# Performance work log

Hardware: AMD Instinct MI355X
Metric: run time of the kernel (lower is better)

Reference implementation:

```python
import jax, jax.numpy as jnp
import numpy as np

NUM_HEADS = 12

def _get_rel_pos(q_size, k_size, rel_pos):
    # rel_pos already has shape (2*max(q,k)-1, head_dim) -> no resize needed
    q_coords = jnp.arange(q_size)[:, None] * max(k_size / q_size, 1.0)
    k_coords = jnp.arange(k_size)[None, :] * max(q_size / k_size, 1.0)
    rel = (q_coords - k_coords + (k_size - 1) * max(q_size / k_size, 1.0)).astype(jnp.int32)
    return rel_pos[rel.reshape(-1)].reshape(q_size, k_size, -1)  # (q, k, head_dim)


def setup_inputs() -> dict:
    key = jax.random.key(0)
    ks = jax.random.split(key, 7)
    B, H, W, C = 1, 64, 64, 768
    head_dim = C // NUM_HEADS
    return {
        "x": jax.random.normal(ks[0], (B, H, W, C), jnp.float32),
        "qkv_w": jax.random.normal(ks[1], (C, 3 * C), jnp.float32) * 0.02,
        "qkv_b": jax.random.normal(ks[2], (3 * C,), jnp.float32) * 0.02,
        "rel_pos_h": jax.random.normal(ks[3], (2 * H - 1, head_dim), jnp.float32) * 0.02,
        "rel_pos_w": jax.random.normal(ks[4], (2 * W - 1, head_dim), jnp.float32) * 0.02,
        "proj_w": jax.random.normal(ks[5], (C, C), jnp.float32) * 0.02,
        "proj_b": jax.random.normal(ks[6], (C,), jnp.float32) * 0.02,
    }


def reference(x, qkv_w, qkv_b, rel_pos_h, rel_pos_w, proj_w, proj_b):
    B, H, W, C = x.shape
    nh = NUM_HEADS
    hd = C // nh
    scale = hd ** (-0.5)
    S = H * W

    qkv = x @ qkv_w + qkv_b                              # (B,H,W,3C)
    qkv = qkv.reshape(B, S, 3, nh, hd).transpose(2, 0, 3, 1, 4).reshape(3, B * nh, S, hd)
    q, k, v = qkv[0], qkv[1], qkv[2]                     # (B*nh, S, hd)

    attn = jnp.einsum('bqd,bkd->bqk', q * scale, k)      # (B*nh, S, S)

    rh = _get_rel_pos(H, H, rel_pos_h)                   # (H,H,hd)
    rw = _get_rel_pos(W, W, rel_pos_w)                   # (W,W,hd)
    r_q = q.reshape(B * nh, H, W, hd)
    rel_h = jnp.einsum('bhwc,hkc->bhwk', r_q, rh)        # (B*nh,H,W,H)
    rel_w = jnp.einsum('bhwc,wkc->bhwk', r_q, rw)        # (B*nh,H,W,W)
    attn = (attn.reshape(B * nh, H, W, H, W)
            + rel_h[:, :, :, :, None]
            + rel_w[:, :, :, None, :]).reshape(B * nh, S, S)

    attn = jax.nn.softmax(attn, axis=-1)
    out = jnp.einsum('bqk,bkd->bqd', attn, v)            # (B*nh, S, hd)
    out = out.reshape(B, nh, H, W, hd).transpose(0, 2, 3, 1, 4).reshape(B, H, W, C)
    return out @ proj_w + proj_b
```

## Files before the change

### kernel.cpp

```cpp
#include <hip/hip_runtime.h>
#include <hip/hip_bf16.h>

#define S_TOK 4096
#define CDIM  768
#define N3C   2304
#define NH    12
#define HD    64

#define LOG2E 1.44269504f

typedef __attribute__((ext_vector_type(8))) short short8;
typedef __attribute__((ext_vector_type(4))) short short4v;
typedef __attribute__((ext_vector_type(4))) float float4v;
typedef __attribute__((ext_vector_type(4))) unsigned uint4v;

__device__ __forceinline__ float b2f(short s) {
    return __uint_as_float(((unsigned)(unsigned short)s) << 16);
}
__device__ __forceinline__ short f2b(float f) {
    unsigned u = __float_as_uint(f);
    unsigned r = (u + 0x7FFFu + ((u >> 16) & 1u)) >> 16;
    return (short)r;
}

#if __has_builtin(__builtin_amdgcn_exp2f)
#define EXP2F __builtin_amdgcn_exp2f
#else
#define EXP2F exp2f
#endif

__device__ __forceinline__ unsigned pack_trunc(float a, float b) {
    return __builtin_amdgcn_perm(__float_as_uint(b), __float_as_uint(a), 0x07060302u);
}

__device__ __forceinline__ short8 u4_to_s8(unsigned a, unsigned b, unsigned c, unsigned d) {
    union { uint4v u; short8 s; } t;
    t.u = (uint4v){a, b, c, d};
    return t.s;
}

__device__ __forceinline__ void load_lds16(const void* g, void* l) {
    __builtin_amdgcn_global_load_lds(
        (const __attribute__((address_space(1))) unsigned int*)g,
        (__attribute__((address_space(3))) unsigned int*)l, 16, 0, 0);
}

__global__ __launch_bounds__(256) void cast_bf16_kernel(
    const float* __restrict__ in, short* __restrict__ out, int n4)
{
    int i = blockIdx.x * 256 + threadIdx.x;
    if (i >= n4) return;
    float4 v = ((const float4*)in)[i];
    short4v o4 = { f2b(v.x), f2b(v.y), f2b(v.z), f2b(v.w) };
    *(short4v*)&out[(size_t)i * 4] = o4;
}

__global__ __launch_bounds__(256) void transpose_cast_kernel(
    const float* __restrict__ in, short* __restrict__ out, int R, int C)
{
    __shared__ float t[64][65];
    const int tid = threadIdx.x;
    const int c0 = blockIdx.x * 64, r0 = blockIdx.y * 64;
    const int li = tid >> 6;
    const int lj = tid & 63;
#pragma unroll
    for (int p = 0; p < 16; ++p) {
        int i = p * 4 + li;
        t[i][lj] = in[(size_t)(r0 + i) * C + c0 + lj];
    }
    __syncthreads();
#pragma unroll
    for (int p = 0; p < 16; ++p) {
        int i = p * 4 + li;
        out[(size_t)(c0 + i) * R + r0 + lj] = f2b(t[lj][i]);
    }
}

#define GEMM_CORE(A_, Bt_)                                                     \
    __shared__ __align__(16) short a_s[128][72];                               \
    __shared__ __align__(16) short b_s[128][72];                               \
    const int tid  = threadIdx.x;                                              \
    const int m0 = blockIdx.y * 128;                                           \
    const int n0 = blockIdx.x * 128;                                           \
    const int lane = tid & 63, w = tid >> 6;                                   \
    const int l15 = lane & 15, quad = lane >> 4;                               \
    const int wr = w >> 1, wc = w & 1;                                         \
    const int srow = tid >> 1;                                                 \
    const int scol = (tid & 1) * 32;                                           \
    float4v acc[4][4];                                                         \
    _Pragma("unroll")                                                          \
    for (int i = 0; i < 4; ++i)                                                \
        _Pragma("unroll")                                                      \
        for (int j = 0; j < 4; ++j) acc[i][j] = (float4v){0.f,0.f,0.f,0.f};    \
    for (int k0 = 0; k0 < 768; k0 += 64) {                                     \
        __syncthreads();                                                       \
        const short* ga = A_ + (size_t)(m0 + srow) * 768 + k0 + scol;          \
        const short* gb = Bt_ + (size_t)(n0 + srow) * 768 + k0 + scol;         \
        _Pragma("unroll")                                                      \
        for (int v = 0; v < 4; ++v) {                                          \
            *(uint4*)&a_s[srow][scol + v*8] = *(const uint4*)(ga + v*8);       \
            *(uint4*)&b_s[srow][scol + v*8] = *(const uint4*)(gb + v*8);       \
        }                                                                      \
        __syncthreads();                                                       \
        _Pragma("unroll")                                                      \
        for (int kk = 0; kk < 64; kk += 32) {                                  \
            short8 af[4], bfr[4];                                              \
            _Pragma("unroll")                                                  \
            for (int i = 0; i < 4; ++i)                                        \
                af[i] = *(const short8*)&a_s[wr*64 + i*16 + l15][kk + quad*8]; \
            _Pragma("unroll")                                                  \
            for (int j = 0; j < 4; ++j)                                        \
                bfr[j] = *(const short8*)&b_s[wc*64 + j*16 + l15][kk + quad*8];\
            _Pragma("unroll")                                                  \
            for (int i = 0; i < 4; ++i)                                        \
                _Pragma("unroll")                                              \
                for (int j = 0; j < 4; ++j)                                    \
                    acc[i][j] = __builtin_amdgcn_mfma_f32_16x16x32_bf16(       \
                        af[i], bfr[j], acc[i][j], 0, 0, 0);                    \
        }                                                                      \
    }

__global__ __launch_bounds__(256) void gemm_qkv_mfma(
    const short* __restrict__ A, const short* __restrict__ Bt,
    const float* __restrict__ bias,
    short* __restrict__ Qb, short* __restrict__ Kb, short* __restrict__ Vt)
{
    GEMM_CORE(A, Bt)

    const int sec = n0 / CDIM;
    float bj[4];
#pragma unroll
    for (int j = 0; j < 4; ++j) bj[j] = bias[n0 + wc*64 + j*16 + l15];

    if (sec < 2) {
        short* dst = (sec == 0) ? Qb : Kb;
#pragma unroll
        for (int i = 0; i < 4; ++i)
#pragma unroll
            for (int j = 0; j < 4; ++j) {
                const int nn = (n0 + wc*64 + j*16 + l15) % CDIM;
                const int head = nn >> 6, d = nn & 63;
#pragma unroll
                for (int r = 0; r < 4; ++r) {
                    const int s = m0 + wr*64 + i*16 + quad*4 + r;
                    dst[((size_t)head * S_TOK + s) * HD + d] = f2b(acc[i][j][r] + bj[j]);
                }
            }
    } else {
#pragma unroll
        for (int i = 0; i < 4; ++i)
#pragma unroll
            for (int j = 0; j < 4; ++j) {
                const int nn = (n0 + wc*64 + j*16 + l15) % CDIM;
                const int head = nn >> 6, d = nn & 63;
                const int sbase = m0 + wr*64 + i*16 + quad*4;
                short4v v4;
#pragma unroll
                for (int r = 0; r < 4; ++r) v4[r] = f2b(acc[i][j][r] + bj[j]);
                *(short4v*)&Vt[((size_t)head * HD + d) * S_TOK + sbase] = v4;
            }
    }
}

__global__ __launch_bounds__(256) void gemm_proj_mfma(
    const short* __restrict__ A, const short* __restrict__ Bt,
    const float* __restrict__ bias, float* __restrict__ out)
{
    GEMM_CORE(A, Bt)

    float bj[4];
#pragma unroll
    for (int j = 0; j < 4; ++j) bj[j] = bias[n0 + wc*64 + j*16 + l15];

#pragma unroll
    for (int i = 0; i < 4; ++i)
#pragma unroll
        for (int j = 0; j < 4; ++j) {
            const int n = n0 + wc*64 + j*16 + l15;
#pragma unroll
            for (int r = 0; r < 4; ++r) {
                const int s = m0 + wr*64 + i*16 + quad*4 + r;
                out[(size_t)s * CDIM + n] = acc[i][j][r] + bj[j];
            }
        }
}

__global__ __launch_bounds__(256) void rel_mfma_kernel(
    const short* __restrict__ Qb, const float* __restrict__ rph,
    const float* __restrict__ rpw, short* __restrict__ Relh,
    short* __restrict__ Relw)
{
    __shared__ __align__(16) short q_s [64][72];
    __shared__ __align__(16) short rh_s[64][72];
    __shared__ __align__(16) short rw_s[128][72];

    const int tid  = threadIdx.x;
    const int y    = blockIdx.x;
    const int head = blockIdx.y;
    const int s0   = y * 64;
    const int w = tid >> 6, lane = tid & 63;
    const int l15 = lane & 15, quad = lane >> 4;
    const int srow = tid >> 2;
    const int scol = (tid & 3) << 4;

    {
        const uint4* g = (const uint4*)(Qb + ((size_t)head * S_TOK + s0 + srow) * HD + scol);
        *(uint4*)&q_s[srow][scol]     = g[0];
        *(uint4*)&q_s[srow][scol + 8] = g[1];
    }
    {
        const float* g = rph + (size_t)(y + srow) * HD + scol;
        short tmp[16];
#pragma unroll
        for (int i = 0; i < 16; i += 4) {
            float4 v = *(const float4*)(g + i);
            tmp[i] = f2b(v.x); tmp[i+1] = f2b(v.y); tmp[i+2] = f2b(v.z); tmp[i+3] = f2b(v.w);
        }
        *(short8*)&rh_s[srow][scol]     = *(short8*)&tmp[0];
        *(short8*)&rh_s[srow][scol + 8] = *(short8*)&tmp[8];
    }
#pragma unroll
    for (int half = 0; half < 2; ++half) {
        const int row = srow + half * 64;
        const int rr  = row > 126 ? 126 : row;
        const float* g = rpw + (size_t)rr * HD + scol;
        short tmp[16];
#pragma unroll
        for (int i = 0; i < 16; i += 4) {
            float4 v = *(const float4*)(g + i);
            tmp[i] = f2b(v.x); tmp[i+1] = f2b(v.y); tmp[i+2] = f2b(v.z); tmp[i+3] = f2b(v.w);
        }
        *(short8*)&rw_s[row][scol]     = *(short8*)&tmp[0];
        *(short8*)&rw_s[row][scol + 8] = *(short8*)&tmp[8];
    }
    __syncthreads();

    const short8 qa0 = *(const short8*)&q_s[w * 16 + l15][quad * 8];
    const short8 qa1 = *(const short8*)&q_s[w * 16 + l15][32 + quad * 8];

#pragma unroll
    for (int ct = 0; ct < 4; ++ct) {
        const int jj = ct * 16 + l15;
        short8 b0 = *(const short8*)&rh_s[jj][quad * 8];
        short8 b1 = *(const short8*)&rh_s[jj][32 + quad * 8];
        float4v z = (float4v){0.f, 0.f, 0.f, 0.f};
        z = __builtin_amdgcn_mfma_f32_16x16x32_bf16(qa0, b0, z, 0, 0, 0);
        z = __builtin_amdgcn_mfma_f32_16x16x32_bf16(qa1, b1, z, 0, 0, 0);
        const int ky = 63 - jj;
#pragma unroll
        for (int r = 0; r < 4; ++r) {
            const int q = w * 16 + quad * 4 + r;
            Relh[((size_t)head * S_TOK + s0 + q) * HD + ky] = f2b(z[r] * LOG2E);
        }
    }

#pragma unroll
    for (int ct = 0; ct < 8; ++ct) {
        const int j = ct * 16 + l15;
        short8 b0 = *(const short8*)&rw_s[j][quad * 8];
        short8 b1 = *(const short8*)&rw_s[j][32 + quad * 8];
        float4v z = (float4v){0.f, 0.f, 0.f, 0.f};
        z = __builtin_amdgcn_mfma_f32_16x16x32_bf16(qa0, b0, z, 0, 0, 0);
        z = __builtin_amdgcn_mfma_f32_16x16x32_bf16(qa1, b1, z, 0, 0, 0);
#pragma unroll
        for (int r = 0; r < 4; ++r) {
            const int q  = w * 16 + quad * 4 + r;
            const int kx = q + 63 - j;
            if (kx >= 0 && kx < 64)
                Relw[((size_t)head * S_TOK + s0 + q) * HD + kx] = f2b(z[r] * LOG2E);
        }
    }
}

__global__ __launch_bounds__(256, 3) void flash_kernel(
    const short* __restrict__ Qb, const short* __restrict__ Kb,
    const short* __restrict__ Vt, const short* __restrict__ Relh,
    const short* __restrict__ Relw, short* __restrict__ attn_b)
{
    __shared__ __align__(16) short lds_s[24576];

    const int tid  = threadIdx.x;
    const int head = blockIdx.y;
    const int s0   = blockIdx.x * 64;
    const int w    = tid >> 6, lane = tid & 63;
    const int l15  = lane & 15, quad = lane >> 4;
    const int ph   = w >> 1;
    const int qh   = w & 1;

    const float C1 = 0.125f * LOG2E;

    const int lj = lane >> 3;
    const int sl = (lane & 7) ^ lj;
    const int kf0 = (lj & 3) + ((lj & 4) << 1) + qh * 32;

    const short* pKs = Kb + (size_t)head * S_TOK * HD
                     + (size_t)(ph * 32 * 64 + kf0) * HD + sl * 8;
    const short* pVs = Vt + ((size_t)head * HD + qh * 32 + lj) * S_TOK
                     + ph * 32 * 64 + sl * 8;

    short* lk0 = &lds_s[(ph * 2 + 0) << 12] + qh * 32 * 64;
    short* lk1 = &lds_s[(ph * 2 + 1) << 12] + qh * 32 * 64;
    short* lv  = &lds_s[16384 + (ph << 12)] + qh * 32 * 64;
    const short* krd0 = &lds_s[(ph * 2 + 0) << 12];
    const short* krd1 = &lds_s[(ph * 2 + 1) << 12];
    const short* vrd  = &lds_s[16384 + (ph << 12)];

    const int roff0 = (quad ^ (l15 & 7)) << 4;
    const int roff1 = roff0 ^ 64;

    short8 qb[2][2];
#pragma unroll
    for (int qt = 0; qt < 2; ++qt) {
        const short* qrow = Qb + ((size_t)head * S_TOK + s0 + qh * 32 + qt * 16 + l15) * HD;
        qb[qt][0] = *(const short8*)(qrow + quad * 8);
        qb[qt][1] = *(const short8*)(qrow + 32 + quad * 8);
    }

    float rwv[2][4][4];
#pragma unroll
    for (int qt = 0; qt < 2; ++qt) {
        const short* rwrow = Relw + ((size_t)head * S_TOK + s0 + qh * 32 + qt * 16 + l15) * HD;
#pragma unroll
        for (int kt = 0; kt < 4; ++kt) {
            const int base = ((kt & 1) << 2) | ((kt >> 1) << 5);
            short4v v = *(const short4v*)(rwrow + base + quad * 8);
#pragma unroll
            for (int r = 0; r < 4; ++r) rwv[qt][kt][r] = b2f(v[r]);
        }
    }

    const short* rhrow0 = Relh + ((size_t)head * S_TOK + s0 + qh * 32 + l15) * HD;
    const short* rhrow1 = rhrow0 + 16 * HD;

    short8 aones;
#pragma unroll
    for (int j = 0; j < 8; ++j) aones[j] = (short)0x3F80;

    float4v od[2][4];
#pragma unroll
    for (int qt = 0; qt < 2; ++qt)
#pragma unroll
        for (int dt = 0; dt < 4; ++dt) od[qt][dt] = (float4v){0.f, 0.f, 0.f, 0.f};
    float4v dq0 = (float4v){0.f, 0.f, 0.f, 0.f};
    float4v dq1 = (float4v){0.f, 0.f, 0.f, 0.f};

    load_lds16(pKs,        lk0);
    load_lds16(pKs + 1024, lk0 + 8  * 64);
    load_lds16(pKs + 256,  lk0 + 16 * 64);
    load_lds16(pKs + 1280, lk0 + 24 * 64);
    __syncthreads();

    for (int t = 0; t < 32; ++t) {
        const int cur = t & 1;
        const short* krd = cur ? krd1 : krd0;
        short* lkn = cur ? lk0 : lk1;

        load_lds16(pVs,               lv);
        load_lds16(pVs + 8  * S_TOK,  lv + 8  * 64);
        load_lds16(pVs + 16 * S_TOK,  lv + 16 * 64);
        load_lds16(pVs + 24 * S_TOK,  lv + 24 * 64);
        if (t < 31) {
            const short* pk = pKs + 4096;
            load_lds16(pk,        lkn);
            load_lds16(pk + 1024, lkn + 8  * 64);
            load_lds16(pk + 256,  lkn + 16 * 64);
            load_lds16(pk + 1280, lkn + 24 * 64);
        }
        pKs += 4096;
        pVs += 64;

        const int c = ph * 32 + t;
        const float rhc0 = b2f(rhrow0[c]);
        const float rhc1 = b2f(rhrow1[c]);

        unsigned pkk[2][8];
#pragma unroll
        for (int kt = 0; kt < 4; ++kt) {
            const char* krp = (const char*)(krd + (kt * 16 + l15) * 64);
            const short8 ka0 = *(const short8*)(krp + roff0);
            const short8 ka1 = *(const short8*)(krp + roff1);
            {
                float4v z = (float4v){0.f, 0.f, 0.f, 0.f};
                z = __builtin_amdgcn_mfma_f32_16x16x32_bf16(ka0, qb[0][0], z, 0, 0, 0);
                z = __builtin_amdgcn_mfma_f32_16x16x32_bf16(ka1, qb[0][1], z, 0, 0, 0);
                float p0 = EXP2F(C1 * z[0] + (rhc0 + rwv[0][kt][0]));
                float p1 = EXP2F(C1 * z[1] + (rhc0 + rwv[0][kt][1]));
                float p2 = EXP2F(C1 * z[2] + (rhc0 + rwv[0][kt][2]));
                float p3 = EXP2F(C1 * z[3] + (rhc0 + rwv[0][kt][3]));
                pkk[0][kt * 2]     = pack_trunc(p0, p1);
                pkk[0][kt * 2 + 1] = pack_trunc(p2, p3);
            }
            {
                float4v z = (float4v){0.f, 0.f, 0.f, 0.f};
                z = __builtin_amdgcn_mfma_f32_16x16x32_bf16(ka0, qb[1][0], z, 0, 0, 0);
                z = __builtin_amdgcn_mfma_f32_16x16x32_bf16(ka1, qb[1][1], z, 0, 0, 0);
                float p0 = EXP2F(C1 * z[0] + (rhc1 + rwv[1][kt][0]));
                float p1 = EXP2F(C1 * z[1] + (rhc1 + rwv[1][kt][1]));
                float p2 = EXP2F(C1 * z[2] + (rhc1 + rwv[1][kt][2]));
                float p3 = EXP2F(C1 * z[3] + (rhc1 + rwv[1][kt][3]));
                pkk[1][kt * 2]     = pack_trunc(p0, p1);
                pkk[1][kt * 2 + 1] = pack_trunc(p2, p3);
            }
        }
        const short8 pb00 = u4_to_s8(pkk[0][0], pkk[0][1], pkk[0][2], pkk[0][3]);
        const short8 pb01 = u4_to_s8(pkk[0][4], pkk[0][5], pkk[0][6], pkk[0][7]);
        const short8 pb10 = u4_to_s8(pkk[1][0], pkk[1][1], pkk[1][2], pkk[1][3]);
        const short8 pb11 = u4_to_s8(pkk[1][4], pkk[1][5], pkk[1][6], pkk[1][7]);

        __syncthreads();

#pragma unroll
        for (int dt = 0; dt < 4; ++dt) {
            const char* vrp = (const char*)(vrd + (dt * 16 + l15) * 64);
            const short8 va0 = *(const short8*)(vrp + roff0);
            const short8 va1 = *(const short8*)(vrp + roff1);
            od[0][dt] = __builtin_amdgcn_mfma_f32_16x16x32_bf16(va0, pb00, od[0][dt], 0, 0, 0);
            od[0][dt] = __builtin_amdgcn_mfma_f32_16x16x32_bf16(va1, pb01, od[0][dt], 0, 0, 0);
            od[1][dt] = __builtin_amdgcn_mfma_f32_16x16x32_bf16(va0, pb10, od[1][dt], 0, 0, 0);
            od[1][dt] = __builtin_amdgcn_mfma_f32_16x16x32_bf16(va1, pb11, od[1][dt], 0, 0, 0);
        }
        dq0 = __builtin_amdgcn_mfma_f32_16x16x32_bf16(aones, pb00, dq0, 0, 0, 0);
        dq0 = __builtin_amdgcn_mfma_f32_16x16x32_bf16(aones, pb01, dq0, 0, 0, 0);
        dq1 = __builtin_amdgcn_mfma_f32_16x16x32_bf16(aones, pb10, dq1, 0, 0, 0);
        dq1 = __builtin_amdgcn_mfma_f32_16x16x32_bf16(aones, pb11, dq1, 0, 0, 0);

        __syncthreads();
    }

    float* cf = (float*)lds_s;
    if (ph == 1) {
#pragma unroll
        for (int qt = 0; qt < 2; ++qt)
#pragma unroll
            for (int dt = 0; dt < 4; ++dt) {
                float* dst = &cf[((((qh * 2 + qt) * 4 + dt) * 16) + quad * 4) * 16 + l15];
#pragma unroll
                for (int r = 0; r < 4; ++r) dst[r * 16] = od[qt][dt][r];
            }
        if (quad == 0) {
            cf[4096 + (qh * 2 + 0) * 16 + l15] = dq0[0];
            cf[4096 + (qh * 2 + 1) * 16 + l15] = dq1[0];
        }
    }
    __syncthreads();
    if (ph == 0) {
#pragma unroll
        for (int qt = 0; qt < 2; ++qt) {
            const float dtot = ((qt == 0) ? dq0[0] : dq1[0])
                             + cf[4096 + (qh * 2 + qt) * 16 + l15];
            const float inv = 1.f / dtot;
            short* outp = attn_b + (size_t)(s0 + qh * 32 + qt * 16 + l15) * CDIM + head * HD;
#pragma unroll
            for (int dt = 0; dt < 4; ++dt) {
                const float* src = &cf[((((qh * 2 + qt) * 4 + dt) * 16) + quad * 4) * 16 + l15];
                short4v o4;
#pragma unroll
                for (int r = 0; r < 4; ++r)
                    o4[r] = f2b((od[qt][dt][r] + src[r * 16]) * inv);
                *(short4v*)(outp + dt * 16 + quad * 4) = o4;
            }
        }
    }
}

extern "C" void kernel_launch(void* const* d_in, const int* in_sizes, int n_in,
                              void* d_out, int out_size, void* d_ws, size_t ws_size,
                              hipStream_t stream)
{
    const float* x    = (const float*)d_in[0];
    const float* qkvw = (const float*)d_in[1];
    const float* qkvb = (const float*)d_in[2];
    const float* rph  = (const float*)d_in[3];
    const float* rpw  = (const float*)d_in[4];
    const float* pw   = (const float*)d_in[5];
    const float* pb   = (const float*)d_in[6];
    float* out = (float*)d_out;

    const size_t HSD = (size_t)NH * S_TOK * HD;
    short* xb     = (short*)d_ws;
    short* wt     = xb + (size_t)S_TOK * CDIM;
    short* pwt    = wt + (size_t)N3C * CDIM;
    short* Qb     = pwt + (size_t)CDIM * CDIM;
    short* Kb     = Qb + HSD;
    short* Vt     = Kb + HSD;
    short* Relh   = Vt + HSD;
    short* Relw   = Relh + HSD;
    short* attn_b = Relw + HSD;

    cast_bf16_kernel<<<S_TOK * CDIM / 4 / 256, 256, 0, stream>>>(x, xb, S_TOK * CDIM / 4);
    transpose_cast_kernel<<<dim3(N3C / 64, CDIM / 64), 256, 0, stream>>>(qkvw, wt, CDIM, N3C);
    transpose_cast_kernel<<<dim3(CDIM / 64, CDIM / 64), 256, 0, stream>>>(pw, pwt, CDIM, CDIM);

    gemm_qkv_mfma<<<dim3(N3C / 128, S_TOK / 128), 256, 0, stream>>>(
        xb, wt, qkvb, Qb, Kb, Vt);
    rel_mfma_kernel<<<dim3(64, NH), 256, 0, stream>>>(Qb, rph, rpw, Relh, Relw);
    flash_kernel<<<dim3(64, NH), 256, 0, stream>>>(Qb, Kb, Vt, Relh, Relw, attn_b);
    gemm_proj_mfma<<<dim3(CDIM / 128, S_TOK / 128), 256, 0, stream>>>(
        attn_b, pwt, pb, out);
}
```

Measured before the change: 224.2 us.

## Use direct-to-LDS swizzled GEMM loads, transpose Relh, prefetch bias, set MFMA priority

The shared GEMM core now fills LDS with direct global-to-LDS 16-byte loads (load_lds16) into an unpadded tile, using an XOR swizzle on the read offsets to avoid bank conflicts. The rel kernel writes the height bias transposed (head, ky, token), so it can store vectorized 4-element chunks. The flash kernel prefetches the next iteration's height-bias value so the load overlaps the current tile's compute. It also raises wave priority around the PV MFMA block. This mixes several independent changes, and correctness depends on the load_lds16 helper and the swizzle mapping matching the read side.

```diff
diff --git a/kernel.cpp b/kernel.cpp
--- a/kernel.cpp
+++ b/kernel.cpp
@@ -77,16 +77,22 @@
 }
 
 #define GEMM_CORE(A_, Bt_)                                                     \
-    __shared__ __align__(16) short a_s[128][72];                               \
-    __shared__ __align__(16) short b_s[128][72];                               \
+    __shared__ __align__(16) short a_s[128][64];                               \
+    __shared__ __align__(16) short b_s[128][64];                               \
     const int tid  = threadIdx.x;                                              \
     const int m0 = blockIdx.y * 128;                                           \
     const int n0 = blockIdx.x * 128;                                           \
     const int lane = tid & 63, w = tid >> 6;                                   \
     const int l15 = lane & 15, quad = lane >> 4;                               \
     const int wr = w >> 1, wc = w & 1;                                         \
-    const int srow = tid >> 1;                                                 \
-    const int scol = (tid & 1) * 32;                                           \
+    const int roff0 = (quad ^ (l15 & 7)) << 4;                                 \
+    const int roff1 = roff0 ^ 64;                                              \
+    const int srow0 = w * 8 + (lane >> 3);                                     \
+    const int sslot = (lane & 7) ^ ((lane >> 3) & 7);                          \
+    const short* ga = A_ + (size_t)(m0 + srow0) * 768 + sslot * 8;             \
+    const short* gb = Bt_ + (size_t)(n0 + srow0) * 768 + sslot * 8;            \
+    short* la = &a_s[w * 8][0];                                                \
+    short* lb = &b_s[w * 8][0];                                                \
     float4v acc[4][4];                                                         \
     _Pragma("unroll")                                                          \
     for (int i = 0; i < 4; ++i)                                                \
@@ -94,23 +100,22 @@
         for (int j = 0; j < 4; ++j) acc[i][j] = (float4v){0.f,0.f,0.f,0.f};    \
     for (int k0 = 0; k0 < 768; k0 += 64) {                                     \
         __syncthreads();                                                       \
-        const short* ga = A_ + (size_t)(m0 + srow) * 768 + k0 + scol;          \
-        const short* gb = Bt_ + (size_t)(n0 + srow) * 768 + k0 + scol;         \
         _Pragma("unroll")                                                      \
-        for (int v = 0; v < 4; ++v) {                                          \
-            *(uint4*)&a_s[srow][scol + v*8] = *(const uint4*)(ga + v*8);       \
-            *(uint4*)&b_s[srow][scol + v*8] = *(const uint4*)(gb + v*8);       \
+        for (int i = 0; i < 4; ++i) {                                          \
+            load_lds16(ga + (size_t)i * (32 * 768) + k0, la + i * 32 * 64);    \
+            load_lds16(gb + (size_t)i * (32 * 768) + k0, lb + i * 32 * 64);    \
         }                                                                      \
         __syncthreads();                                                       \
         _Pragma("unroll")                                                      \
         for (int kk = 0; kk < 64; kk += 32) {                                  \
+            const int roff = kk ? roff1 : roff0;                               \
             short8 af[4], bfr[4];                                              \
             _Pragma("unroll")                                                  \
             for (int i = 0; i < 4; ++i)                                        \
-                af[i] = *(const short8*)&a_s[wr*64 + i*16 + l15][kk + quad*8]; \
+                af[i] = *(const short8*)((const char*)&a_s[wr*64 + i*16 + l15][0] + roff); \
             _Pragma("unroll")                                                  \
             for (int j = 0; j < 4; ++j)                                        \
-                bfr[j] = *(const short8*)&b_s[wc*64 + j*16 + l15][kk + quad*8];\
+                bfr[j] = *(const short8*)((const char*)&b_s[wc*64 + j*16 + l15][0] + roff); \
             _Pragma("unroll")                                                  \
             for (int i = 0; i < 4; ++i)                                        \
                 _Pragma("unroll")                                              \
@@ -187,7 +192,7 @@
 
 __global__ __launch_bounds__(256) void rel_mfma_kernel(
     const short* __restrict__ Qb, const float* __restrict__ rph,
-    const float* __restrict__ rpw, short* __restrict__ Relh,
+    const float* __restrict__ rpw, short* __restrict__ RelhT,
     short* __restrict__ Relw)
 {
     __shared__ __align__(16) short q_s [64][72];
@@ -247,11 +252,10 @@
         z = __builtin_amdgcn_mfma_f32_16x16x32_bf16(qa0, b0, z, 0, 0, 0);
         z = __builtin_amdgcn_mfma_f32_16x16x32_bf16(qa1, b1, z, 0, 0, 0);
         const int ky = 63 - jj;
-#pragma unroll
-        for (int r = 0; r < 4; ++r) {
-            const int q = w * 16 + quad * 4 + r;
-            Relh[((size_t)head * S_TOK + s0 + q) * HD + ky] = f2b(z[r] * LOG2E);
-        }
+        short4v o4;
+#pragma unroll
+        for (int r = 0; r < 4; ++r) o4[r] = f2b(z[r] * LOG2E);
+        *(short4v*)&RelhT[((size_t)head * HD + ky) * S_TOK + s0 + w * 16 + quad * 4] = o4;
     }
 
 #pragma unroll
@@ -274,7 +278,7 @@
 
 __global__ __launch_bounds__(256, 3) void flash_kernel(
     const short* __restrict__ Qb, const short* __restrict__ Kb,
-    const short* __restrict__ Vt, const short* __restrict__ Relh,
+    const short* __restrict__ Vt, const short* __restrict__ RelhT,
     const short* __restrict__ Relw, short* __restrict__ attn_b)
 {
     __shared__ __align__(16) short lds_s[24576];
@@ -329,8 +333,9 @@
         }
     }
 
-    const short* rhrow0 = Relh + ((size_t)head * S_TOK + s0 + qh * 32 + l15) * HD;
-    const short* rhrow1 = rhrow0 + 16 * HD;
+    const short* rhbase = RelhT + (size_t)head * HD * S_TOK + s0 + qh * 32 + l15;
+    float rhc0 = b2f(rhbase[(size_t)(ph * 32) * S_TOK]);
+    float rhc1 = b2f(rhbase[(size_t)(ph * 32) * S_TOK + 16]);
 
     short8 aones;
 #pragma unroll
@@ -369,9 +374,11 @@
         pKs += 4096;
         pVs += 64;
 
-        const int c = ph * 32 + t;
-        const float rhc0 = b2f(rhrow0[c]);
-        const float rhc1 = b2f(rhrow1[c]);
+        short rhn0, rhn1;
+        if (t < 31) {
+            rhn0 = rhbase[(size_t)(ph * 32 + t + 1) * S_TOK];
+            rhn1 = rhbase[(size_t)(ph * 32 + t + 1) * S_TOK + 16];
+        }
 
         unsigned pkk[2][8];
 #pragma unroll
@@ -409,6 +416,7 @@
 
         __syncthreads();
 
+        __builtin_amdgcn_s_setprio(1);
 #pragma unroll
         for (int dt = 0; dt < 4; ++dt) {
             const char* vrp = (const char*)(vrd + (dt * 16 + l15) * 64);
@@ -423,7 +431,12 @@
         dq0 = __builtin_amdgcn_mfma_f32_16x16x32_bf16(aones, pb01, dq0, 0, 0, 0);
         dq1 = __builtin_amdgcn_mfma_f32_16x16x32_bf16(aones, pb10, dq1, 0, 0, 0);
         dq1 = __builtin_amdgcn_mfma_f32_16x16x32_bf16(aones, pb11, dq1, 0, 0, 0);
-
+        __builtin_amdgcn_s_setprio(0);
+
+        if (t < 31) {
+            rhc0 = b2f(rhn0);
+            rhc1 = b2f(rhn1);
+        }
         __syncthreads();
     }
 
@@ -483,8 +496,8 @@
     short* Qb     = pwt + (size_t)CDIM * CDIM;
     short* Kb     = Qb + HSD;
     short* Vt     = Kb + HSD;
-    short* Relh   = Vt + HSD;
-    short* Relw   = Relh + HSD;
+    short* RelhT  = Vt + HSD;
+    short* Relw   = RelhT + HSD;
     short* attn_b = Relw + HSD;
 
     cast_bf16_kernel<<<S_TOK * CDIM / 4 / 256, 256, 0, stream>>>(x, xb, S_TOK * CDIM / 4);
@@ -493,8 +506,8 @@
 
     gemm_qkv_mfma<<<dim3(N3C / 128, S_TOK / 128), 256, 0, stream>>>(
         xb, wt, qkvb, Qb, Kb, Vt);
-    rel_mfma_kernel<<<dim3(64, NH), 256, 0, stream>>>(Qb, rph, rpw, Relh, Relw);
-    flash_kernel<<<dim3(64, NH), 256, 0, stream>>>(Qb, Kb, Vt, Relh, Relw, attn_b);
+    rel_mfma_kernel<<<dim3(64, NH), 256, 0, stream>>>(Qb, rph, rpw, RelhT, Relw);
+    flash_kernel<<<dim3(64, NH), 256, 0, stream>>>(Qb, Kb, Vt, RelhT, Relw, attn_b);
     gemm_proj_mfma<<<dim3(CDIM / 128, S_TOK / 128), 256, 0, stream>>>(
         attn_b, pwt, pb, out);
 }
```

After: 209.6 us. -6.5%, faster.
